# Performance work log

Measured on AMD Instinct MI355X. Metric: run time of the kernel, lower is better.

The kernel has to match this reference:

```python
import jax, jax.numpy as jnp
import numpy as np

NUM_NODES = 2048
EMB = (512, 512, 256)
LATENT = 512
N_FEAT = 512
N_TOTAL = 16384  # batch_size * NUM_NODES
N_EDGES = 524288


def setup_inputs() -> dict:
    key = jax.random.key(0)
    ks = jax.random.split(key, 14)
    s = 0.02
    inp = {
        "x": jax.random.normal(ks[0], (N_TOTAL, N_FEAT), jnp.float32),
        "edge_index": jax.random.randint(ks[1], (2, N_EDGES), 0, N_TOTAL, dtype=jnp.int64),
        "batch_size": 8,
        "batch_index": jax.random.randint(ks[2], (N_TOTAL,), 0, 8, dtype=jnp.int64),
        "W1": jax.random.normal(ks[3], (N_FEAT, EMB[0]), jnp.float32) * s,
        "b1": jnp.zeros((EMB[0],), jnp.float32),
        "W2": jax.random.normal(ks[4], (EMB[0], EMB[1]), jnp.float32) * s,
        "b2": jnp.zeros((EMB[1],), jnp.float32),
        "W3": jax.random.normal(ks[5], (EMB[1], EMB[2]), jnp.float32) * s,
        "b3": jnp.zeros((EMB[2],), jnp.float32),
        "We": jax.random.normal(ks[6], (NUM_NODES * EMB[2], LATENT), jnp.float32) * s,
        "be": jnp.zeros((LATENT,), jnp.float32),
        "Wd": jax.random.normal(ks[7], (LATENT, NUM_NODES), jnp.float32) * s,
        "bd": jnp.zeros((NUM_NODES,), jnp.float32),
    }
    return inp


def reference(x, edge_index, batch_size, batch_index, W1, b1, W2, b2, W3, b3, We, be, Wd, bd):
    N = x.shape[0]
    loops = jnp.arange(N)
    row = jnp.concatenate([edge_index[0], loops])  # sources
    col = jnp.concatenate([edge_index[1], loops])  # targets
    # symmetric degree normalization (PyG GCNConv with self loops)
    deg = jax.ops.segment_sum(jnp.ones_like(col, dtype=x.dtype), col, num_segments=N)
    dinv = jnp.where(deg > 0, jax.lax.rsqrt(deg), jnp.zeros_like(deg))
    norm = (dinv[row] * dinv[col])[:, None]  # [E+N, 1]

    def gcn(h, W, b):
        h = h @ W  # transform first (PyG order)
        return jax.ops.segment_sum(h[row] * norm, col, num_segments=N) + b

    h = jax.nn.relu(gcn(x, W1, b1))
    h = jax.nn.relu(gcn(h, W2, b2))
    h = gcn(h, W3, b3)                      # [N, EMB[2]]
    h = h.reshape(-1, NUM_NODES * EMB[2])   # [batch, NUM_NODES*EMB[2]]
    z = h @ We + be                          # encoder Linear
    out = z @ Wd + bd                        # decoder Linear -> [batch, NUM_NODES]
    return out
```

## Files before the change

### kernel.cpp

```cpp
#include <hip/hip_runtime.h>
#include <stdint.h>

#define NT 16384
#define NN 2048
#define NB 8
#define NBKT 16

typedef __attribute__((ext_vector_type(4))) float f32x4;
typedef __attribute__((ext_vector_type(2))) float f32x2;
typedef __attribute__((ext_vector_type(8))) short s16x8;
typedef __attribute__((ext_vector_type(4))) short s16x4;

__device__ __forceinline__ float bf2f(short u) {
    unsigned v = ((unsigned)(unsigned short)u) << 16;
    return __builtin_bit_cast(float, v);
}
__device__ __forceinline__ short f2bf(float f) {
    unsigned u = __builtin_bit_cast(unsigned, f);
    u += 0x7fffu + ((u >> 16) & 1u);
    return (short)(u >> 16);
}
__device__ __forceinline__ void gload16(const void* g, void* l) {
    __builtin_amdgcn_global_load_lds(
        (const __attribute__((address_space(1))) void*)g,
        (__attribute__((address_space(3))) void*)l, 16, 0, 0);
}
__device__ __forceinline__ long long eidx(const void* ei, long long i, int is64) {
    if (is64) return ((const long long*)ei)[i];
    return (long long)((const int*)ei)[i];
}

__global__ void k_detect(const void* ei, int nchk, int* flag) {
    __shared__ int bad;
    if (threadIdx.x == 0) bad = 0;
    __syncthreads();
    const long long* p = (const long long*)ei;
    for (int i = threadIdx.x; i < nchk; i += 256) {
        long long v = p[i];
        if (v < 0 || v >= NT) bad = 1;
    }
    __syncthreads();
    if (threadIdx.x == 0) *flag = bad ? 0 : 1;
}

__global__ void k_count16(const void* ei, int E, const int* flag, int* cnt16) {
    int e = blockIdx.x * 256 + threadIdx.x;
    if (e >= E) return;
    int f = *flag;
    int r = (int)eidx(ei, e, f);
    int c = (int)eidx(ei, (long long)E + e, f);
    atomicAdd(&cnt16[c * NBKT + (r >> 10)], 1);
}

__global__ void k_deg(const int* __restrict__ cnt16, int* __restrict__ deg) {
    int n = blockIdx.x * 256 + threadIdx.x;
    const int* p = cnt16 + n * NBKT;
    int s = 0;
#pragma unroll
    for (int j = 0; j < NBKT; j++) s += p[j];
    deg[n] = s;
}

__global__ __launch_bounds__(1024) void k_scan(const int* __restrict__ count,
        int* __restrict__ offs, float* __restrict__ dinv) {
    __shared__ int ps[1024];
    const int t = threadIdx.x;
    const int base = t * 16;
    int loc[16];
    int s = 0;
#pragma unroll
    for (int j = 0; j < 16; j++) { loc[j] = count[base + j]; s += loc[j]; }
    ps[t] = s;
    __syncthreads();
    for (int o = 1; o < 1024; o <<= 1) {
        int v = (t >= o) ? ps[t - o] : 0;
        __syncthreads();
        ps[t] += v;
        __syncthreads();
    }
    int ex = ps[t] - s;
#pragma unroll
    for (int j = 0; j < 16; j++) {
        offs[base + j] = ex;
        ex += loc[j];
        dinv[base + j] = rsqrtf((float)(loc[j] + 1));
    }
}

__global__ void k_bcur(const int* __restrict__ cnt16, const int* __restrict__ offs,
                       int* __restrict__ bcur) {
    int n = blockIdx.x * 256 + threadIdx.x;
    int running = offs[n];
#pragma unroll
    for (int b = 0; b < NBKT; b++) {
        bcur[n * NBKT + b] = running;
        running += cnt16[n * NBKT + b];
    }
}

__global__ void k_fill16(const void* ei, int E, const int* flag,
                         int* bcur, int* csr) {
    int e = blockIdx.x * 256 + threadIdx.x;
    if (e >= E) return;
    int f = *flag;
    int r = (int)eidx(ei, e, f);
    int c = (int)eidx(ei, (long long)E + e, f);
    int pos = atomicAdd(&bcur[c * NBKT + (r >> 10)], 1);
    csr[pos] = r;
}

__global__ void k_convw_all(const float* __restrict__ W1, const float* __restrict__ W2,
                            const float* __restrict__ W3, short* __restrict__ Wt1,
                            short* __restrict__ Wt2, short* __restrict__ Wt3) {
    int idx = blockIdx.x * 256 + threadIdx.x;
    const float* W; short* Wt; int N, base;
    if (idx < 262144)      { W = W1; Wt = Wt1; N = 512; base = idx; }
    else if (idx < 524288) { W = W2; Wt = Wt2; N = 512; base = idx - 262144; }
    else                   { W = W3; Wt = Wt3; N = 256; base = idx - 524288; }
    int k = base / N, n = base - k * N;
    Wt[(size_t)n * 512 + k] = f2bf(W[base]);
}

__global__ __launch_bounds__(256) void k_scale_x(const float* __restrict__ x,
        const float* __restrict__ dinv, short* __restrict__ xs) {
    int i = blockIdx.x * 256 + threadIdx.x;
    f32x4 v = *(const f32x4*)(x + (size_t)i * 4);
    float d = dinv[i >> 7];
    s16x4 o;
#pragma unroll
    for (int j = 0; j < 4; j++) o[j] = f2bf(v[j] * d);
    *(s16x4*)(xs + (size_t)i * 4) = o;
}

__global__ __launch_bounds__(256) void k_gemm(const short* __restrict__ A,
        const short* __restrict__ Bt, short* __restrict__ Co, int N, int K) {
    __shared__ short As[4096];
    __shared__ short Bs[4096];
    const int t = threadIdx.x;
    const int w = t >> 6, l = t & 63;
    const int row0 = blockIdx.x * 128;
    const int col0 = blockIdx.y * 128;
    const int lr = l & 15, lhi = l >> 4;
    const int wr = (w >> 1) * 64, wc = (w & 1) * 64;
    const int srow = t >> 2;
    const int skoff = (t & 3) * 8;
    const int ldsbase = w * 512;
    f32x4 acc[4][4] = {};
    for (int k0 = 0; k0 < K; k0 += 32) {
#pragma unroll
        for (int i = 0; i < 2; i++) {
            int r = i * 64 + srow;
            gload16(A  + (size_t)(row0 + r) * K + k0 + skoff, (void*)(As + i * 2048 + ldsbase));
            gload16(Bt + (size_t)(col0 + r) * K + k0 + skoff, (void*)(Bs + i * 2048 + ldsbase));
        }
        __syncthreads();
        s16x8 af[4], bfr[4];
#pragma unroll
        for (int m = 0; m < 4; m++) af[m]  = *(const s16x8*)(As + (wr + m * 16 + lr) * 32 + lhi * 8);
#pragma unroll
        for (int n = 0; n < 4; n++) bfr[n] = *(const s16x8*)(Bs + (wc + n * 16 + lr) * 32 + lhi * 8);
#pragma unroll
        for (int m = 0; m < 4; m++)
#pragma unroll
            for (int n = 0; n < 4; n++)
                acc[m][n] = __builtin_amdgcn_mfma_f32_16x16x32_bf16(af[m], bfr[n], acc[m][n], 0, 0, 0);
        __syncthreads();
    }
#pragma unroll
    for (int m = 0; m < 4; m++)
#pragma unroll
        for (int n = 0; n < 4; n++)
#pragma unroll
            for (int j = 0; j < 4; j++) {
                int r = row0 + wr + m * 16 + lhi * 4 + j;
                int c = col0 + wc + n * 16 + lr;
                Co[(size_t)r * N + c] = f2bf(acc[m][n][j]);
            }
}

__global__ __launch_bounds__(256) void k_agg512(const short* __restrict__ T,
        const int* __restrict__ offs, const int* __restrict__ cnt,
        const int* __restrict__ csr, const float* __restrict__ dinv,
        const float* __restrict__ bias, short* __restrict__ H) {
    const int w = threadIdx.x >> 6, l = threadIdx.x & 63;
    const int node = blockIdx.x * 4 + w;
    const int c0 = l * 8;
    const short* base = T + c0;
    float acc[8];
    {
        s16x8 r = *(const s16x8*)(base + (size_t)node * 512);
#pragma unroll
        for (int v = 0; v < 8; v++) acc[v] = bf2f(r[v]);
    }
    const int beg = offs[node], end = beg + cnt[node];
    int j = beg;
    for (; j + 8 <= end; j += 8) {
        int sIx[8];
#pragma unroll
        for (int q = 0; q < 8; q++) sIx[q] = csr[j + q];
        s16x8 r[8];
#pragma unroll
        for (int q = 0; q < 8; q++) r[q] = *(const s16x8*)(base + (size_t)sIx[q] * 512);
#pragma unroll
        for (int v = 0; v < 8; v++) {
            float s01 = bf2f(r[0][v]) + bf2f(r[1][v]);
            float s23 = bf2f(r[2][v]) + bf2f(r[3][v]);
            float s45 = bf2f(r[4][v]) + bf2f(r[5][v]);
            float s67 = bf2f(r[6][v]) + bf2f(r[7][v]);
            acc[v] += (s01 + s23) + (s45 + s67);
        }
    }
    for (; j + 2 <= end; j += 2) {
        int s0 = csr[j], s1 = csr[j + 1];
        s16x8 r0 = *(const s16x8*)(base + (size_t)s0 * 512);
        s16x8 r1 = *(const s16x8*)(base + (size_t)s1 * 512);
#pragma unroll
        for (int v = 0; v < 8; v++) acc[v] += bf2f(r0[v]) + bf2f(r1[v]);
    }
    for (; j < end; j++) {
        s16x8 r0 = *(const s16x8*)(base + (size_t)csr[j] * 512);
#pragma unroll
        for (int v = 0; v < 8; v++) acc[v] += bf2f(r0[v]);
    }
    const float dc = dinv[node];
    f32x4 b0 = *(const f32x4*)(bias + c0);
    f32x4 b1 = *(const f32x4*)(bias + c0 + 4);
    s16x8 outv;
#pragma unroll
    for (int v = 0; v < 8; v++) {
        float bb = (v < 4) ? b0[v] : b1[v - 4];
        float o = acc[v] * dc + bb;
        o = fmaxf(o, 0.f);
        o *= dc;
        outv[v] = f2bf(o);
    }
    *(s16x8*)(H + (size_t)node * 512 + c0) = outv;
}

__global__ __launch_bounds__(256) void k_agg256(const short* __restrict__ T,
        const int* __restrict__ offs, const int* __restrict__ cnt,
        const int* __restrict__ csr, const float* __restrict__ dinv,
        const float* __restrict__ bias, float* __restrict__ H3) {
    const int w = threadIdx.x >> 6, l = threadIdx.x & 63;
    const int node = blockIdx.x * 4 + w;
    const int c0 = l * 4;
    const short* base = T + c0;
    float acc[4];
    {
        s16x4 r = *(const s16x4*)(base + (size_t)node * 256);
#pragma unroll
        for (int v = 0; v < 4; v++) acc[v] = bf2f(r[v]);
    }
    const int beg = offs[node], end = beg + cnt[node];
    int j = beg;
    for (; j + 8 <= end; j += 8) {
        int sIx[8];
#pragma unroll
        for (int q = 0; q < 8; q++) sIx[q] = csr[j + q];
        s16x4 r[8];
#pragma unroll
        for (int q = 0; q < 8; q++) r[q] = *(const s16x4*)(base + (size_t)sIx[q] * 256);
#pragma unroll
        for (int v = 0; v < 4; v++) {
            float s01 = bf2f(r[0][v]) + bf2f(r[1][v]);
            float s23 = bf2f(r[2][v]) + bf2f(r[3][v]);
            float s45 = bf2f(r[4][v]) + bf2f(r[5][v]);
            float s67 = bf2f(r[6][v]) + bf2f(r[7][v]);
            acc[v] += (s01 + s23) + (s45 + s67);
        }
    }
    for (; j < end; j++) {
        s16x4 r0 = *(const s16x4*)(base + (size_t)csr[j] * 256);
#pragma unroll
        for (int v = 0; v < 4; v++) acc[v] += bf2f(r0[v]);
    }
    const float dc = dinv[node];
    f32x4 bb = *(const f32x4*)(bias + c0);
    f32x4 o;
#pragma unroll
    for (int v = 0; v < 4; v++) o[v] = acc[v] * dc + bb[v];
    *(f32x4*)(H3 + (size_t)node * 256 + c0) = o;
}

__global__ __launch_bounds__(256) void k_enc(const float* __restrict__ h3,
        const float* __restrict__ We, float* __restrict__ part) {
    __shared__ float hT[512 * 8];
    __shared__ float red[32 * 128];
    const int t = threadIdx.x;
    const int k0 = blockIdx.x * 512;
    for (int i = t; i < 4096; i += 256) {
        int b = i >> 9, k = i & 511;
        hT[k * 8 + b] = h3[(size_t)b * 524288 + k0 + k];
    }
    __syncthreads();
    const int col = (t & 127) * 4;
    const int khalf = t >> 7;
    float acc[8][4] = {};
    const float* wp = We + (size_t)(k0 + khalf * 256) * 512 + col;
    const float* hp = hT + khalf * 256 * 8;
#pragma unroll 2
    for (int k = 0; k < 256; k++) {
        f32x4 wv = *(const f32x4*)(wp + (size_t)k * 512);
        f32x4 ha = *(const f32x4*)(hp + k * 8);
        f32x4 hb = *(const f32x4*)(hp + k * 8 + 4);
#pragma unroll
        for (int c = 0; c < 4; c++) {
            acc[0][c] += ha[0] * wv[c];
            acc[1][c] += ha[1] * wv[c];
            acc[2][c] += ha[2] * wv[c];
            acc[3][c] += ha[3] * wv[c];
            acc[4][c] += hb[0] * wv[c];
            acc[5][c] += hb[1] * wv[c];
            acc[6][c] += hb[2] * wv[c];
            acc[7][c] += hb[3] * wv[c];
        }
    }
    if (khalf) {
#pragma unroll
        for (int b = 0; b < 8; b++)
#pragma unroll
            for (int c = 0; c < 4; c++)
                red[(b * 4 + c) * 128 + (t - 128)] = acc[b][c];
    }
    __syncthreads();
    if (!khalf) {
#pragma unroll
        for (int b = 0; b < 8; b++) {
            f32x4 o;
#pragma unroll
            for (int c = 0; c < 4; c++) o[c] = acc[b][c] + red[(b * 4 + c) * 128 + t];
            *(f32x4*)(part + (size_t)blockIdx.x * 4096 + b * 512 + col) = o;
        }
    }
}

__global__ __launch_bounds__(256) void k_zred(const float* __restrict__ part,
                                              float* __restrict__ zpart) {
    const int n = blockIdx.x * 256 + threadIdx.x;
    const int p0 = blockIdx.y * 128;
    float s = 0.f;
    for (int q = 0; q < 128; q++) s += part[(size_t)(p0 + q) * 4096 + n];
    zpart[(size_t)blockIdx.y * 4096 + n] = s;
}

__global__ __launch_bounds__(256) void k_dec(const float* __restrict__ zpart,
        const float* __restrict__ be, const float* __restrict__ Wd,
        const float* __restrict__ bd, float* __restrict__ out) {
    __shared__ float zs[512];
    const int b = blockIdx.x >> 3;
    const int n = ((blockIdx.x & 7) << 8) + threadIdx.x;
    for (int i = threadIdx.x; i < 512; i += 256) {
        float s = be[i];
#pragma unroll
        for (int p = 0; p < 8; p++) s += zpart[(size_t)p * 4096 + b * 512 + i];
        zs[i] = s;
    }
    __syncthreads();
    float acc = bd[n];
    for (int k = 0; k < 512; k++) acc += zs[k] * Wd[(size_t)k * 2048 + n];
    out[b * 2048 + n] = acc;
}

extern "C" void kernel_launch(void* const* d_in, const int* in_sizes, int n_in,
                              void* d_out, int out_size, void* d_ws, size_t ws_size,
                              hipStream_t stream) {
    const float* x  = (const float*)d_in[0];
    const void*  ei = d_in[1];
    const float* W1 = (const float*)d_in[4];
    const float* b1 = (const float*)d_in[5];
    const float* W2 = (const float*)d_in[6];
    const float* b2 = (const float*)d_in[7];
    const float* W3 = (const float*)d_in[8];
    const float* b3 = (const float*)d_in[9];
    const float* We = (const float*)d_in[10];
    const float* be = (const float*)d_in[11];
    const float* Wd = (const float*)d_in[12];
    const float* bd = (const float*)d_in[13];
    float* out = (float*)d_out;
    const int E = in_sizes[1] / 2;

    char* ws = (char*)d_ws;
    size_t off = 0;
    auto alloc = [&](size_t bytes) {
        void* p = ws + off;
        off = (off + bytes + 255) & ~(size_t)255;
        return p;
    };
    int*   flag   = (int*)  alloc(4);
    int*   deg    = (int*)  alloc((size_t)NT * 4);
    int*   offs   = (int*)  alloc((size_t)NT * 4);
    float* dinv   = (float*)alloc((size_t)NT * 4);
    int*   csr    = (int*)  alloc((size_t)E * 4);
    short* Wt1    = (short*)alloc((size_t)512 * 512 * 2);
    short* Wt2    = (short*)alloc((size_t)512 * 512 * 2);
    short* Wt3    = (short*)alloc((size_t)256 * 512 * 2);
    short* bufA   = (short*)alloc((size_t)NT * 512 * 2);
    short* bufB   = (short*)alloc((size_t)NT * 512 * 2);
    float* part   = (float*)alloc((size_t)1024 * 4096 * 4);
    float* zpart  = (float*)alloc((size_t)8 * 4096 * 4);
    int*   cnt16  = (int*)part;
    int*   bcur   = ((int*)part) + NT * NBKT;

    hipMemsetAsync(cnt16, 0, (size_t)NT * NBKT * 4, stream);

    k_detect<<<1, 256, 0, stream>>>(ei, 2048, flag);
    k_count16<<<(E + 255) / 256, 256, 0, stream>>>(ei, E, flag, cnt16);
    k_deg<<<NT / 256, 256, 0, stream>>>(cnt16, deg);
    k_scan<<<1, 1024, 0, stream>>>(deg, offs, dinv);
    k_bcur<<<NT / 256, 256, 0, stream>>>(cnt16, offs, bcur);
    k_fill16<<<(E + 255) / 256, 256, 0, stream>>>(ei, E, flag, bcur, csr);

    k_convw_all<<<2560, 256, 0, stream>>>(W1, W2, W3, Wt1, Wt2, Wt3);
    k_scale_x<<<(NT * 512 / 4) / 256, 256, 0, stream>>>(x, dinv, bufA);

    dim3 g1(128, 4);
    k_gemm<<<g1, 256, 0, stream>>>(bufA, Wt1, bufB, 512, 512);
    k_agg512<<<NT / 4, 256, 0, stream>>>(bufB, offs, deg, csr, dinv, b1, bufA);
    k_gemm<<<g1, 256, 0, stream>>>(bufA, Wt2, bufB, 512, 512);
    k_agg512<<<NT / 4, 256, 0, stream>>>(bufB, offs, deg, csr, dinv, b2, bufA);
    dim3 g3(128, 2);
    k_gemm<<<g3, 256, 0, stream>>>(bufA, Wt3, bufB, 256, 512);
    k_agg256<<<NT / 4, 256, 0, stream>>>(bufB, offs, deg, csr, dinv, b3, (float*)bufA);

    k_enc<<<1024, 256, 0, stream>>>((const float*)bufA, We, part);
    dim3 gz(16, 8);
    k_zred<<<gz, 256, 0, stream>>>(part, zpart);
    k_dec<<<64, 256, 0, stream>>>(zpart, be, Wd, bd, out);
}
```

Measured before the change: 516.9 us.

## Retile GEMM to 64x128 blocks with K=64 steps and XOR-swizzled LDS

The bf16 MFMA GEMM moves from 128x128 tiles with K-step 32 to 64x128 tiles with K-step 64. Each wave now computes a 64x32 slice, and the grid doubles to 256 row blocks. LDS rows are XOR-swizzled to avoid bank conflicts, and launch bounds request 4 blocks per CU. The aim is more blocks in flight to fill the CUs, fewer barriers per K, and conflict-free fragment reads, at the cost of less reuse of each A/B load per block.

```diff
diff --git a/kernel.cpp b/kernel.cpp
--- a/kernel.cpp
+++ b/kernel.cpp
@@ -132,47 +132,74 @@
     *(s16x4*)(xs + (size_t)i * 4) = o;
 }
 
-__global__ __launch_bounds__(256) void k_gemm(const short* __restrict__ A,
+__global__ __launch_bounds__(256, 4) void k_gemm(const short* __restrict__ A,
         const short* __restrict__ Bt, short* __restrict__ Co, int N, int K) {
-    __shared__ short As[4096];
-    __shared__ short Bs[4096];
+    __shared__ short As[64 * 64];
+    __shared__ short Bs[128 * 64];
     const int t = threadIdx.x;
     const int w = t >> 6, l = t & 63;
-    const int row0 = blockIdx.x * 128;
+    const int row0 = blockIdx.x * 64;
     const int col0 = blockIdx.y * 128;
     const int lr = l & 15, lhi = l >> 4;
-    const int wr = (w >> 1) * 64, wc = (w & 1) * 64;
-    const int srow = t >> 2;
-    const int skoff = (t & 3) * 8;
-    const int ldsbase = w * 512;
-    f32x4 acc[4][4] = {};
-    for (int k0 = 0; k0 < K; k0 += 32) {
-#pragma unroll
-        for (int i = 0; i < 2; i++) {
-            int r = i * 64 + srow;
-            gload16(A  + (size_t)(row0 + r) * K + k0 + skoff, (void*)(As + i * 2048 + ldsbase));
-            gload16(Bt + (size_t)(col0 + r) * K + k0 + skoff, (void*)(Bs + i * 2048 + ldsbase));
-        }
+    const int wc = w * 32;
+    f32x4 acc[4][2] = {};
+    int arow[2], ajs[2], brow[4], bjs[4];
+#pragma unroll
+    for (int i = 0; i < 2; i++) {
+        int s = t + i * 256;
+        arow[i] = s >> 3; ajs[i] = (s & 7) ^ (arow[i] & 7);
+    }
+#pragma unroll
+    for (int i = 0; i < 4; i++) {
+        int s = t + i * 256;
+        brow[i] = s >> 3; bjs[i] = (s & 7) ^ (brow[i] & 7);
+    }
+    int aoff[2][4], boff[2][2];
+#pragma unroll
+    for (int kk = 0; kk < 2; kk++) {
+#pragma unroll
+        for (int m = 0; m < 4; m++) {
+            int ar = m * 16 + lr;
+            aoff[kk][m] = ar * 64 + (((kk * 4 + lhi) ^ (ar & 7)) << 3);
+        }
+#pragma unroll
+        for (int n = 0; n < 2; n++) {
+            int br = wc + n * 16 + lr;
+            boff[kk][n] = br * 64 + (((kk * 4 + lhi) ^ (br & 7)) << 3);
+        }
+    }
+    for (int k0 = 0; k0 < K; k0 += 64) {
+#pragma unroll
+        for (int i = 0; i < 2; i++)
+            gload16(A + (size_t)(row0 + arow[i]) * K + k0 + ajs[i] * 8,
+                    (void*)(As + (t + i * 256) * 8));
+#pragma unroll
+        for (int i = 0; i < 4; i++)
+            gload16(Bt + (size_t)(col0 + brow[i]) * K + k0 + bjs[i] * 8,
+                    (void*)(Bs + (t + i * 256) * 8));
         __syncthreads();
-        s16x8 af[4], bfr[4];
-#pragma unroll
-        for (int m = 0; m < 4; m++) af[m]  = *(const s16x8*)(As + (wr + m * 16 + lr) * 32 + lhi * 8);
-#pragma unroll
-        for (int n = 0; n < 4; n++) bfr[n] = *(const s16x8*)(Bs + (wc + n * 16 + lr) * 32 + lhi * 8);
-#pragma unroll
-        for (int m = 0; m < 4; m++)
-#pragma unroll
-            for (int n = 0; n < 4; n++)
-                acc[m][n] = __builtin_amdgcn_mfma_f32_16x16x32_bf16(af[m], bfr[n], acc[m][n], 0, 0, 0);
+#pragma unroll
+        for (int kk = 0; kk < 2; kk++) {
+            s16x8 af[4], bfr[2];
+#pragma unroll
+            for (int m = 0; m < 4; m++) af[m]  = *(const s16x8*)(As + aoff[kk][m]);
+#pragma unroll
+            for (int n = 0; n < 2; n++) bfr[n] = *(const s16x8*)(Bs + boff[kk][n]);
+#pragma unroll
+            for (int m = 0; m < 4; m++)
+#pragma unroll
+                for (int n = 0; n < 2; n++)
+                    acc[m][n] = __builtin_amdgcn_mfma_f32_16x16x32_bf16(af[m], bfr[n], acc[m][n], 0, 0, 0);
+        }
         __syncthreads();
     }
 #pragma unroll
     for (int m = 0; m < 4; m++)
 #pragma unroll
-        for (int n = 0; n < 4; n++)
+        for (int n = 0; n < 2; n++)
 #pragma unroll
             for (int j = 0; j < 4; j++) {
-                int r = row0 + wr + m * 16 + lhi * 4 + j;
+                int r = row0 + m * 16 + lhi * 4 + j;
                 int c = col0 + wc + n * 16 + lr;
                 Co[(size_t)r * N + c] = f2bf(acc[m][n][j]);
             }
@@ -413,12 +440,12 @@
     k_convw_all<<<2560, 256, 0, stream>>>(W1, W2, W3, Wt1, Wt2, Wt3);
     k_scale_x<<<(NT * 512 / 4) / 256, 256, 0, stream>>>(x, dinv, bufA);
 
-    dim3 g1(128, 4);
+    dim3 g1(256, 4);
     k_gemm<<<g1, 256, 0, stream>>>(bufA, Wt1, bufB, 512, 512);
     k_agg512<<<NT / 4, 256, 0, stream>>>(bufB, offs, deg, csr, dinv, b1, bufA);
     k_gemm<<<g1, 256, 0, stream>>>(bufA, Wt2, bufB, 512, 512);
     k_agg512<<<NT / 4, 256, 0, stream>>>(bufB, offs, deg, csr, dinv, b2, bufA);
-    dim3 g3(128, 2);
+    dim3 g3(256, 2);
     k_gemm<<<g3, 256, 0, stream>>>(bufA, Wt3, bufB, 256, 512);
     k_agg256<<<NT / 4, 256, 0, stream>>>(bufB, offs, deg, csr, dinv, b3, (float*)bufA);
 
```

Measured after the change: 505.5 us. 2.2% less time.
